# Performance work log

Measured on AMD Instinct MI355X. Metric: run time of the kernel, lower is better.

## Reference

```python
import jax, jax.numpy as jnp
import numpy as np

N = 200000
E = 3200000
F_IN = 128
D = 64
G = 512
T = 10


def setup_inputs() -> dict:
    key = jax.random.key(0)
    ks = jax.random.split(key, 20)
    def lin(k, out_d, in_d):
        kw, kb = jax.random.split(k)
        s = 1.0 / np.sqrt(in_d)
        W = jax.random.uniform(kw, (out_d, in_d), jnp.float32, -s, s)
        b = jax.random.uniform(kb, (out_d,), jnp.float32, -s, s)
        return W, b
    x = jax.random.normal(ks[0], (N, F_IN), jnp.float32)
    edge_index = jax.random.randint(ks[1], (2, E), 0, N, jnp.int32)
    batch = jnp.sort(jax.random.randint(ks[2], (N,), 0, G, jnp.int32))
    Wc0, bc0 = lin(ks[3], D, F_IN)
    Wc1, bc1 = lin(ks[4], D, D)
    Wc2, bc2 = lin(ks[5], D, D)
    Wc3, bc3 = lin(ks[6], D, D)
    Wmax, bmax = lin(ks[7], D, D)
    W1, b1 = lin(ks[8], D, 4 * D)
    W2, b2 = lin(ks[9], T, D)
    return {"x": x, "edge_index": edge_index, "batch": batch, "num_graphs": G,
            "Wc0": Wc0, "bc0": bc0, "Wc1": Wc1, "bc1": bc1,
            "Wc2": Wc2, "bc2": bc2, "Wc3": Wc3, "bc3": bc3,
            "Wmax": Wmax, "bmax": bmax, "W1": W1, "b1": b1, "W2": W2, "b2": b2}


def gcn_conv(x, W, b, src, dst, n):
    # PyG GCNConv: h = x W^T; add self-loops; sym-normalize by (deg+1)^-1/2
    h = x @ W.T  # [n, D]
    deg = jax.ops.segment_sum(jnp.ones_like(dst, jnp.float32), dst, num_segments=n) + 1.0
    dis = deg ** -0.5  # deg >= 1 always (self loop)
    coef = (dis[src] * dis[dst])[:, None]  # [E,1]
    agg = jax.ops.segment_sum(h[src] * coef, dst, num_segments=n)
    agg = agg + h * (dis * dis)[:, None]  # self-loop contribution
    return agg + b


def reference(x, edge_index, batch, num_graphs,
              Wc0, bc0, Wc1, bc1, Wc2, bc2, Wc3, bc3,
              Wmax, bmax, W1, b1, W2, b2):
    n = x.shape[0]
    src, dst = edge_index[0], edge_index[1]
    convs = [(Wc0, bc0), (Wc1, bc1), (Wc2, bc2), (Wc3, bc3)]
    h = x
    h_all = []
    for (W, b) in convs:
        h = gcn_conv(h, W, b, src, dst, n)
        h = jax.nn.relu(h @ Wmax.T + bmax)
        h_all.append(h)
    hcat = jnp.concatenate(h_all, axis=1)  # [n, 4*D]
    pooled = jax.ops.segment_max(hcat, batch, num_segments=num_graphs)
    pooled = jnp.where(jnp.isfinite(pooled), pooled, 0.0)  # empty graphs -> 0
    out = jax.nn.relu(pooled @ W1.T + b1)
    return out @ W2.T + b2
```

## Files before the change

kernel.cpp:

```cpp
#include <hip/hip_runtime.h>
#include <hip/hip_bf16.h>
#include <math.h>

constexpr int N_NODES = 200000;
constexpr int E_EDGES = 3200000;
constexpr int F_IN    = 128;
constexpr int D       = 64;
constexpr int G_GRAPHS = 512;
constexpr int T_OUT   = 10;

constexpr int SCAN_CHUNK   = 2048;
constexpr int SCAN_NBLOCKS = (N_NODES + SCAN_CHUNK - 1) / SCAN_CHUNK;

constexpr int NPASS = 4;
constexpr int PASS_RANGE = N_NODES / NPASS;

__global__ __launch_bounds__(256) void deg_pass(const int* __restrict__ dst,
                                                int* __restrict__ deg,
                                                int lo, int hi) {
    int e0 = (blockIdx.x * 256 + threadIdx.x) * 4;
    if (e0 >= E_EDGES) return;
    int4 d4 = *(const int4*)(dst + e0);
    const int* dp = (const int*)&d4;
    #pragma unroll
    for (int i = 0; i < 4; ++i) {
        int d = dp[i];
        if (d >= lo && d < hi) atomicAdd(&deg[d], 1);
    }
}

__global__ __launch_bounds__(256) void dis_kernel(const int* __restrict__ deg,
                                                  float* __restrict__ dis) {
    int i = blockIdx.x * 256 + threadIdx.x;
    if (i < N_NODES) dis[i] = 1.0f / sqrtf((float)deg[i] + 1.0f);
}

__global__ __launch_bounds__(256) void scan_p1(const int* __restrict__ deg,
                                               int* __restrict__ bsum) {
    const int b = blockIdx.x, t = threadIdx.x;
    int idx0 = b * SCAN_CHUNK + t * 8;
    int s = 0;
    #pragma unroll
    for (int i = 0; i < 8; ++i) {
        int idx = idx0 + i;
        if (idx < N_NODES) s += deg[idx];
    }
    #pragma unroll
    for (int off = 32; off; off >>= 1) s += __shfl_down(s, off, 64);
    __shared__ int ws[4];
    if ((t & 63) == 0) ws[t >> 6] = s;
    __syncthreads();
    if (t == 0) bsum[b] = ws[0] + ws[1] + ws[2] + ws[3];
}

__global__ __launch_bounds__(128) void scan_p2(int* __restrict__ bsum,
                                               int* __restrict__ row_ptr) {
    __shared__ int tmp[128];
    const int t = threadIdx.x;
    int v = (t < SCAN_NBLOCKS) ? bsum[t] : 0;
    tmp[t] = v;
    __syncthreads();
    #pragma unroll
    for (int off = 1; off < 128; off <<= 1) {
        int u = (t >= off) ? tmp[t - off] : 0;
        __syncthreads();
        tmp[t] += u;
        __syncthreads();
    }
    if (t < SCAN_NBLOCKS) bsum[t] = tmp[t] - v;
    if (t == 0) row_ptr[N_NODES] = E_EDGES;
}

__global__ __launch_bounds__(256) void scan_p3(const int* __restrict__ deg,
                                               const int* __restrict__ bsum,
                                               int* __restrict__ row_ptr) {
    const int b = blockIdx.x, t = threadIdx.x;
    int idx0 = b * SCAN_CHUNK + t * 8;
    int loc[8];
    int s = 0;
    #pragma unroll
    for (int i = 0; i < 8; ++i) {
        int idx = idx0 + i;
        loc[i] = (idx < N_NODES) ? deg[idx] : 0;
        s += loc[i];
    }
    __shared__ int tmp[256];
    tmp[t] = s;
    __syncthreads();
    #pragma unroll
    for (int off = 1; off < 256; off <<= 1) {
        int u = (t >= off) ? tmp[t - off] : 0;
        __syncthreads();
        tmp[t] += u;
        __syncthreads();
    }
    int run = tmp[t] - s + bsum[b];
    #pragma unroll
    for (int i = 0; i < 8; ++i) {
        int idx = idx0 + i;
        if (idx < N_NODES) row_ptr[idx] = run;
        run += loc[i];
    }
}

__global__ __launch_bounds__(256) void place_pass(const int* __restrict__ src,
                                                  const int* __restrict__ dst,
                                                  const int* __restrict__ row_ptr,
                                                  int* __restrict__ cursor,
                                                  int* __restrict__ csr_src,
                                                  int lo, int hi) {
    int e0 = (blockIdx.x * 256 + threadIdx.x) * 4;
    if (e0 >= E_EDGES) return;
    int4 d4 = *(const int4*)(dst + e0);
    const int* dp = (const int*)&d4;
    #pragma unroll
    for (int i = 0; i < 4; ++i) {
        int d = dp[i];
        if (d >= lo && d < hi) {
            int pos = row_ptr[d] + atomicAdd(&cursor[d], 1);
            csr_src[pos] = src[e0 + i];
        }
    }
}

__global__ __launch_bounds__(256) void bprime_kernel(const float* __restrict__ Wmax,
                                                     const float* __restrict__ bmax,
                                                     const float* __restrict__ bc0,
                                                     const float* __restrict__ bc1,
                                                     const float* __restrict__ bc2,
                                                     const float* __restrict__ bc3,
                                                     float* __restrict__ bprime) {
    const int l = threadIdx.x >> 6, c = threadIdx.x & 63;
    const float* bc = (l == 0) ? bc0 : (l == 1) ? bc1 : (l == 2) ? bc2 : bc3;
    float s = bmax[c];
    const float* w = Wmax + c * D;
    #pragma unroll
    for (int k = 0; k < D; k += 4) {
        float4 wv = *(const float4*)(w + k);
        float4 bv = *(const float4*)(bc + k);
        s += wv.x * bv.x + wv.y * bv.y + wv.z * bv.z + wv.w * bv.w;
    }
    bprime[l * D + c] = s;
}

template<int K>
__global__ __launch_bounds__(256) void gemm_k(const float* __restrict__ in,
                                              const float* __restrict__ W,
                                              float* __restrict__ out,
                                              const float* __restrict__ dis) {
    constexpr int GPR = K / 4;
    __shared__ float Xs[64 * K];
    __shared__ float Ws[D * K];
    __shared__ float ds[64];
    const int tid = threadIdx.x;
    const size_t row0 = (size_t)blockIdx.x * 64;

    for (int li = tid; li < 64 * GPR; li += 256) {
        int r = li / GPR, g = li % GPR;
        float4 v = *(const float4*)(in + (row0 + r) * K + g * 4);
        int gs = g ^ ((r >> 2) & 7);
        *(float4*)(Xs + r * K + gs * 4) = v;
    }
    for (int li = tid; li < D * GPR; li += 256) {
        int r = li / GPR, g = li % GPR;
        float4 v = *(const float4*)(W + r * K + g * 4);
        int gs = g ^ ((r >> 2) & 7);
        *(float4*)(Ws + r * K + gs * 4) = v;
    }
    if (tid < 64) ds[tid] = dis[row0 + tid];
    __syncthreads();

    const int lane = tid & 63;
    const int wave = tid >> 6;
    const int rg = lane & 15;
    const int cg = wave * 4 + (lane >> 4);
    float acc[4][4] = {};
    #pragma unroll 8
    for (int kq = 0; kq < GPR; ++kq) {
        float4 xv[4], wv[4];
        #pragma unroll
        for (int i = 0; i < 4; ++i)
            xv[i] = *(const float4*)(Xs + (rg * 4 + i) * K + ((kq ^ (rg & 7)) * 4));
        #pragma unroll
        for (int j = 0; j < 4; ++j)
            wv[j] = *(const float4*)(Ws + (cg * 4 + j) * K + ((kq ^ (cg & 7)) * 4));
        #pragma unroll
        for (int i = 0; i < 4; ++i)
            #pragma unroll
            for (int j = 0; j < 4; ++j)
                acc[i][j] += xv[i].x * wv[j].x + xv[i].y * wv[j].y +
                             xv[i].z * wv[j].z + xv[i].w * wv[j].w;
    }
    #pragma unroll
    for (int i = 0; i < 4; ++i) {
        size_t r = row0 + rg * 4 + i;
        float sc = ds[rg * 4 + i];
        float4 o = make_float4(acc[i][0] * sc, acc[i][1] * sc,
                               acc[i][2] * sc, acc[i][3] * sc);
        *(float4*)(out + r * D + cg * 4) = o;
    }
}

template<bool HAS_NEXT>
__global__ __launch_bounds__(256) void fused2_kernel(const float* __restrict__ A,
                                                     const float* __restrict__ Wmax,
                                                     const float* __restrict__ Wcn,
                                                     const float* __restrict__ bprime,
                                                     const int* __restrict__ batch,
                                                     const float* __restrict__ dis,
                                                     int* __restrict__ pooled,
                                                     float* __restrict__ Hout,
                                                     int layer) {
    __shared__ float Xs[64 * D];
    __shared__ float Ws[64 * D];
    __shared__ float Ws2[64 * D];
    __shared__ int   bs[64];
    __shared__ float ds[64];
    __shared__ float bb[64];
    const int tid = threadIdx.x;
    const size_t row0 = (size_t)blockIdx.x * 64;

    for (int li = tid; li < 64 * 16; li += 256) {
        int r = li >> 4, g = li & 15;
        float4 v = *(const float4*)(A + (row0 + r) * D + g * 4);
        *(float4*)(Xs + r * D + ((g ^ ((r >> 2) & 7)) * 4)) = v;
    }
    for (int li = tid; li < 64 * 16; li += 256) {
        int r = li >> 4, g = li & 15;
        float4 v = *(const float4*)(Wmax + r * D + g * 4);
        *(float4*)(Ws + r * D + ((g ^ ((r >> 2) & 7)) * 4)) = v;
    }
    if (HAS_NEXT)
        for (int li = tid; li < 64 * 16; li += 256) {
            int r = li >> 4, g = li & 15;
            float4 v = *(const float4*)(Wcn + r * D + g * 4);
            *(float4*)(Ws2 + r * D + ((g ^ ((r >> 2) & 7)) * 4)) = v;
        }
    if (tid < 64) {
        bs[tid] = batch[row0 + tid];
        bb[tid] = bprime[tid];
        if (HAS_NEXT) ds[tid] = dis[row0 + tid];
    }
    __syncthreads();

    const int lane = tid & 63;
    const int wave = tid >> 6;
    const int rg = lane & 15;
    const int cg = wave * 4 + (lane >> 4);

    float acc[4][4] = {};
    #pragma unroll 8
    for (int kq = 0; kq < 16; ++kq) {
        float4 xv[4], wv[4];
        #pragma unroll
        for (int i = 0; i < 4; ++i)
            xv[i] = *(const float4*)(Xs + (rg * 4 + i) * D + ((kq ^ (rg & 7)) * 4));
        #pragma unroll
        for (int j = 0; j < 4; ++j)
            wv[j] = *(const float4*)(Ws + (cg * 4 + j) * D + ((kq ^ (cg & 7)) * 4));
        #pragma unroll
        for (int i = 0; i < 4; ++i)
            #pragma unroll
            for (int j = 0; j < 4; ++j)
                acc[i][j] += xv[i].x * wv[j].x + xv[i].y * wv[j].y +
                             xv[i].z * wv[j].z + xv[i].w * wv[j].w;
    }

    __syncthreads();
    #pragma unroll
    for (int i = 0; i < 4; ++i) {
        float4 o;
        float* op = (float*)&o;
        #pragma unroll
        for (int j = 0; j < 4; ++j)
            op[j] = fmaxf(acc[i][j] + bb[cg * 4 + j], 0.0f);
        *(float4*)(Xs + (rg * 4 + i) * D + ((cg ^ (rg & 7)) * 4)) = o;
    }
    __syncthreads();

    if (tid < 64) {
        const int col = tid;
        const int cgr = col >> 2, ce = col & 3;
        float m = Xs[(cgr ^ 0) * 4 + ce];
        int bg = bs[0];
        #pragma unroll 8
        for (int r = 1; r < 64; ++r) {
            int b2 = bs[r];
            float v = Xs[r * D + ((cgr ^ ((r >> 2) & 7)) * 4) + ce];
            if (b2 != bg) {
                atomicMax(&pooled[bg * (4 * D) + layer * D + col], __float_as_int(m));
                bg = b2; m = v;
            } else {
                m = fmaxf(m, v);
            }
        }
        atomicMax(&pooled[bg * (4 * D) + layer * D + col], __float_as_int(m));
    }

    if (HAS_NEXT) {
        float acc2[4][4] = {};
        #pragma unroll 8
        for (int kq = 0; kq < 16; ++kq) {
            float4 xv[4], wv[4];
            #pragma unroll
            for (int i = 0; i < 4; ++i)
                xv[i] = *(const float4*)(Xs + (rg * 4 + i) * D + ((kq ^ (rg & 7)) * 4));
            #pragma unroll
            for (int j = 0; j < 4; ++j)
                wv[j] = *(const float4*)(Ws2 + (cg * 4 + j) * D + ((kq ^ (cg & 7)) * 4));
            #pragma unroll
            for (int i = 0; i < 4; ++i)
                #pragma unroll
                for (int j = 0; j < 4; ++j)
                    acc2[i][j] += xv[i].x * wv[j].x + xv[i].y * wv[j].y +
                                  xv[i].z * wv[j].z + xv[i].w * wv[j].w;
        }
        #pragma unroll
        for (int i = 0; i < 4; ++i) {
            size_t r = row0 + rg * 4 + i;
            float sc = ds[rg * 4 + i];
            float4 o = make_float4(acc2[i][0] * sc, acc2[i][1] * sc,
                                   acc2[i][2] * sc, acc2[i][3] * sc);
            *(float4*)(Hout + r * D + cg * 4) = o;
        }
    }
}

__global__ __launch_bounds__(256) void agg_kernel(const int* __restrict__ row_ptr,
                                                  const int* __restrict__ csr_src,
                                                  const float* __restrict__ Lbuf,
                                                  const float* __restrict__ dis,
                                                  float* __restrict__ A) {
    int v = __builtin_amdgcn_readfirstlane((int)(blockIdx.x * 4) + (int)(threadIdx.x >> 6));
    if (v >= N_NODES) return;
    const int lane = threadIdx.x & 63;
    const int beg = row_ptr[v];
    const int end = row_ptr[v + 1];
    float acc = Lbuf[(size_t)v * D + lane];
    #pragma unroll 4
    for (int p = beg; p < end; ++p) {
        int s = csr_src[p];
        acc += Lbuf[(size_t)s * D + lane];
    }
    A[(size_t)v * D + lane] = acc * dis[v];
}

__global__ __launch_bounds__(64) void mlp_kernel(const float* __restrict__ pooled,
                                                 const float* __restrict__ W1,
                                                 const float* __restrict__ b1,
                                                 const float* __restrict__ W2,
                                                 const float* __restrict__ b2,
                                                 float* __restrict__ out) {
    __shared__ float ps[4 * D];
    __shared__ float hs[D];
    const int g = blockIdx.x, t = threadIdx.x;
    *(float4*)(ps + t * 4) = *(const float4*)(pooled + (size_t)g * (4 * D) + t * 4);
    __syncthreads();
    float acc = b1[t];
    const float* w = W1 + (size_t)t * (4 * D);
    #pragma unroll 4
    for (int k = 0; k < 4 * D; k += 4) {
        float4 wv = *(const float4*)(w + k);
        float4 pv = *(const float4*)(ps + k);
        acc += wv.x * pv.x + wv.y * pv.y + wv.z * pv.z + wv.w * pv.w;
    }
    hs[t] = fmaxf(acc, 0.0f);
    __syncthreads();
    if (t < T_OUT) {
        float o = b2[t];
        const float* w2 = W2 + t * D;
        #pragma unroll
        for (int k = 0; k < D; ++k) o += hs[k] * w2[k];
        out[(size_t)g * T_OUT + t] = o;
    }
}

extern "C" void kernel_launch(void* const* d_in, const int* in_sizes, int n_in,
                              void* d_out, int out_size, void* d_ws, size_t ws_size,
                              hipStream_t stream) {
    (void)in_sizes; (void)n_in; (void)out_size; (void)ws_size;
    const float* x     = (const float*)d_in[0];
    const int*   ei    = (const int*)d_in[1];
    const int*   batch = (const int*)d_in[2];
    const float* Wc[4] = {(const float*)d_in[4], (const float*)d_in[6],
                          (const float*)d_in[8], (const float*)d_in[10]};
    const float* bc[4] = {(const float*)d_in[5], (const float*)d_in[7],
                          (const float*)d_in[9], (const float*)d_in[11]};
    const float* Wmax = (const float*)d_in[12];
    const float* bmax = (const float*)d_in[13];
    const float* W1   = (const float*)d_in[14];
    const float* b1   = (const float*)d_in[15];
    const float* W2   = (const float*)d_in[16];
    const float* b2   = (const float*)d_in[17];
    float* out = (float*)d_out;

    float* fws = (float*)d_ws;
    size_t off = 0;
    float* L        = fws + off; off += (size_t)N_NODES * D;
    float* A        = fws + off; off += (size_t)N_NODES * D;
    int*   csr_src  = (int*)(fws + off); off += E_EDGES;
    int*   row_ptr  = (int*)(fws + off); off += N_NODES + 16;
    int*   deg      = (int*)(fws + off); off += N_NODES;
    int*   cursor   = (int*)(fws + off); off += N_NODES;
    float* dis      = fws + off; off += N_NODES;
    int*   pooled   = (int*)(fws + off); off += G_GRAPHS * 4 * D;
    int*   bsum     = (int*)(fws + off); off += SCAN_NBLOCKS + 16;
    float* bprime   = fws + off; off += 4 * D;

    const int* srcI = ei;
    const int* dstI = ei + E_EDGES;

    hipMemsetAsync(deg,    0, sizeof(int) * N_NODES, stream);
    hipMemsetAsync(cursor, 0, sizeof(int) * N_NODES, stream);
    hipMemsetAsync(pooled, 0, sizeof(int) * G_GRAPHS * 4 * D, stream);

    for (int p = 0; p < NPASS; ++p)
        deg_pass<<<E_EDGES / (256 * 4), 256, 0, stream>>>(dstI, deg,
                                                          p * PASS_RANGE,
                                                          (p + 1) * PASS_RANGE);
    dis_kernel<<<(N_NODES + 255) / 256, 256, 0, stream>>>(deg, dis);
    scan_p1<<<SCAN_NBLOCKS, 256, 0, stream>>>(deg, bsum);
    scan_p2<<<1, 128, 0, stream>>>(bsum, row_ptr);
    scan_p3<<<SCAN_NBLOCKS, 256, 0, stream>>>(deg, bsum, row_ptr);
    for (int p = 0; p < NPASS; ++p)
        place_pass<<<E_EDGES / (256 * 4), 256, 0, stream>>>(srcI, dstI, row_ptr,
                                                            cursor, csr_src,
                                                            p * PASS_RANGE,
                                                            (p + 1) * PASS_RANGE);
    bprime_kernel<<<1, 256, 0, stream>>>(Wmax, bmax, bc[0], bc[1], bc[2], bc[3],
                                         bprime);

    gemm_k<F_IN><<<N_NODES / 64, 256, 0, stream>>>(x, Wc[0], L, dis);

    for (int l = 0; l < 4; ++l) {
        agg_kernel<<<N_NODES / 4, 256, 0, stream>>>(row_ptr, csr_src, L, dis, A);
        if (l < 3)
            fused2_kernel<true><<<N_NODES / 64, 256, 0, stream>>>(
                A, Wmax, Wc[l + 1], bprime + l * D, batch, dis, pooled, L, l);
        else
            fused2_kernel<false><<<N_NODES / 64, 256, 0, stream>>>(
                A, Wmax, nullptr, bprime + l * D, batch, nullptr, pooled, nullptr, l);
    }
    mlp_kernel<<<G_GRAPHS, 64, 0, stream>>>((const float*)pooled, W1, b1, W2, b2, out);
}
```

Before: 1.364 ms.

## Fuse CSR neighbor aggregation into per-layer GEMM/pool kernel with ping-pong buffers

Removes the standalone agg_kernel and performs the gather-sum over CSR neighbors inside the fused GEMM/pool kernel, writing aggregated rows directly into shared memory. This drops one full write and read of the N×D intermediate per layer and one kernel launch per layer, and uses two ping-pong buffers for the layer features. It also merges the deg and cursor memsets into one. In exchange, each 256-thread block now serially aggregates 64 nodes (16 per wave) before the GEMM, which lowers parallelism and latency hiding for the irregular gathers compared with the previous one-wave-per-node launch.

```diff
diff --git a/kernel.cpp b/kernel.cpp
--- a/kernel.cpp
+++ b/kernel.cpp
@@ -202,14 +202,16 @@
 }
 
 template<bool HAS_NEXT>
-__global__ __launch_bounds__(256) void fused2_kernel(const float* __restrict__ A,
+__global__ __launch_bounds__(256) void fused3_kernel(const float* __restrict__ Lin,
+                                                     const int* __restrict__ row_ptr,
+                                                     const int* __restrict__ csr_src,
+                                                     const float* __restrict__ dis,
                                                      const float* __restrict__ Wmax,
                                                      const float* __restrict__ Wcn,
                                                      const float* __restrict__ bprime,
                                                      const int* __restrict__ batch,
-                                                     const float* __restrict__ dis,
                                                      int* __restrict__ pooled,
-                                                     float* __restrict__ Hout,
+                                                     float* __restrict__ Lout,
                                                      int layer) {
     __shared__ float Xs[64 * D];
     __shared__ float Ws[64 * D];
@@ -219,12 +221,9 @@
     __shared__ float bb[64];
     const int tid = threadIdx.x;
     const size_t row0 = (size_t)blockIdx.x * 64;
-
-    for (int li = tid; li < 64 * 16; li += 256) {
-        int r = li >> 4, g = li & 15;
-        float4 v = *(const float4*)(A + (row0 + r) * D + g * 4);
-        *(float4*)(Xs + r * D + ((g ^ ((r >> 2) & 7)) * 4)) = v;
-    }
+    const int lane = tid & 63;
+    const int wave = tid >> 6;
+
     for (int li = tid; li < 64 * 16; li += 256) {
         int r = li >> 4, g = li & 15;
         float4 v = *(const float4*)(Wmax + r * D + g * 4);
@@ -241,10 +240,34 @@
         bb[tid] = bprime[tid];
         if (HAS_NEXT) ds[tid] = dis[row0 + tid];
     }
-    __syncthreads();
-
-    const int lane = tid & 63;
-    const int wave = tid >> 6;
+
+    {
+        const int swzg = lane >> 2;
+        const int e    = lane & 3;
+        for (int n = 0; n < 16; ++n) {
+            const int v = wave * 16 + n;
+            const size_t vg = row0 + v;
+            const int beg = row_ptr[vg];
+            const int end = row_ptr[vg + 1];
+            float a = Lin[vg * D + lane];
+            int p = beg;
+            for (; p + 4 <= end; p += 4) {
+                int s0 = csr_src[p + 0], s1 = csr_src[p + 1];
+                int s2 = csr_src[p + 2], s3 = csr_src[p + 3];
+                float r0 = Lin[(size_t)s0 * D + lane];
+                float r1 = Lin[(size_t)s1 * D + lane];
+                float r2 = Lin[(size_t)s2 * D + lane];
+                float r3 = Lin[(size_t)s3 * D + lane];
+                a += r0 + r1 + r2 + r3;
+            }
+            for (; p < end; ++p)
+                a += Lin[(size_t)csr_src[p] * D + lane];
+            a *= dis[vg];
+            Xs[v * D + ((swzg ^ ((v >> 2) & 7)) * 4) + e] = a;
+        }
+    }
+    __syncthreads();
+
     const int rg = lane & 15;
     const int cg = wave * 4 + (lane >> 4);
 
@@ -281,7 +304,7 @@
     if (tid < 64) {
         const int col = tid;
         const int cgr = col >> 2, ce = col & 3;
-        float m = Xs[(cgr ^ 0) * 4 + ce];
+        float m = Xs[cgr * 4 + ce];
         int bg = bs[0];
         #pragma unroll 8
         for (int r = 1; r < 64; ++r) {
@@ -321,28 +344,9 @@
             float sc = ds[rg * 4 + i];
             float4 o = make_float4(acc2[i][0] * sc, acc2[i][1] * sc,
                                    acc2[i][2] * sc, acc2[i][3] * sc);
-            *(float4*)(Hout + r * D + cg * 4) = o;
-        }
-    }
-}
-
-__global__ __launch_bounds__(256) void agg_kernel(const int* __restrict__ row_ptr,
-                                                  const int* __restrict__ csr_src,
-                                                  const float* __restrict__ Lbuf,
-                                                  const float* __restrict__ dis,
-                                                  float* __restrict__ A) {
-    int v = __builtin_amdgcn_readfirstlane((int)(blockIdx.x * 4) + (int)(threadIdx.x >> 6));
-    if (v >= N_NODES) return;
-    const int lane = threadIdx.x & 63;
-    const int beg = row_ptr[v];
-    const int end = row_ptr[v + 1];
-    float acc = Lbuf[(size_t)v * D + lane];
-    #pragma unroll 4
-    for (int p = beg; p < end; ++p) {
-        int s = csr_src[p];
-        acc += Lbuf[(size_t)s * D + lane];
-    }
-    A[(size_t)v * D + lane] = acc * dis[v];
+            *(float4*)(Lout + r * D + cg * 4) = o;
+        }
+    }
 }
 
 __global__ __launch_bounds__(64) void mlp_kernel(const float* __restrict__ pooled,
@@ -396,8 +400,8 @@
 
     float* fws = (float*)d_ws;
     size_t off = 0;
-    float* L        = fws + off; off += (size_t)N_NODES * D;
-    float* A        = fws + off; off += (size_t)N_NODES * D;
+    float* bufA     = fws + off; off += (size_t)N_NODES * D;
+    float* bufB     = fws + off; off += (size_t)N_NODES * D;
     int*   csr_src  = (int*)(fws + off); off += E_EDGES;
     int*   row_ptr  = (int*)(fws + off); off += N_NODES + 16;
     int*   deg      = (int*)(fws + off); off += N_NODES;
@@ -410,8 +414,7 @@
     const int* srcI = ei;
     const int* dstI = ei + E_EDGES;
 
-    hipMemsetAsync(deg,    0, sizeof(int) * N_NODES, stream);
-    hipMemsetAsync(cursor, 0, sizeof(int) * N_NODES, stream);
+    hipMemsetAsync(deg,    0, sizeof(int) * 2 * N_NODES, stream);
     hipMemsetAsync(pooled, 0, sizeof(int) * G_GRAPHS * 4 * D, stream);
 
     for (int p = 0; p < NPASS; ++p)
@@ -430,16 +433,21 @@
     bprime_kernel<<<1, 256, 0, stream>>>(Wmax, bmax, bc[0], bc[1], bc[2], bc[3],
                                          bprime);
 
-    gemm_k<F_IN><<<N_NODES / 64, 256, 0, stream>>>(x, Wc[0], L, dis);
-
+    gemm_k<F_IN><<<N_NODES / 64, 256, 0, stream>>>(x, Wc[0], bufA, dis);
+
+    const float* cur = bufA;
+    float*       nxt = bufB;
     for (int l = 0; l < 4; ++l) {
-        agg_kernel<<<N_NODES / 4, 256, 0, stream>>>(row_ptr, csr_src, L, dis, A);
-        if (l < 3)
-            fused2_kernel<true><<<N_NODES / 64, 256, 0, stream>>>(
-                A, Wmax, Wc[l + 1], bprime + l * D, batch, dis, pooled, L, l);
-        else
-            fused2_kernel<false><<<N_NODES / 64, 256, 0, stream>>>(
-                A, Wmax, nullptr, bprime + l * D, batch, nullptr, pooled, nullptr, l);
+        if (l < 3) {
+            fused3_kernel<true><<<N_NODES / 64, 256, 0, stream>>>(
+                cur, row_ptr, csr_src, dis, Wmax, Wc[l + 1], bprime + l * D,
+                batch, pooled, nxt, l);
+            const float* t = cur; cur = nxt; nxt = (float*)t;
+        } else {
+            fused3_kernel<false><<<N_NODES / 64, 256, 0, stream>>>(
+                cur, row_ptr, csr_src, dis, Wmax, nullptr, bprime + l * D,
+                batch, pooled, nullptr, l);
+        }
     }
     mlp_kernel<<<G_GRAPHS, 64, 0, stream>>>((const float*)pooled, W1, b1, W2, b2, out);
 }
```

After: 1.920 ms. 1.41x slower.
